# Kernel tuning notes

Measured on AMD Instinct MI355X. Metric: run time of the kernel, lower is better.

## Reference

```python
import math
import jax, jax.numpy as jnp
import numpy as np

D_MODEL = 1024
NUM_HEADS = 16
HEAD_DIM = D_MODEL // NUM_HEADS
B, T = 2, 2048


def setup_inputs() -> dict:
    key = jax.random.key(0)
    ks = jax.random.split(key, 11)
    s = 0.02
    inp = {
        'x':  jax.random.normal(ks[0], (B, T, D_MODEL), dtype=jnp.float32),
        'Wq': jax.random.normal(ks[1], (D_MODEL, D_MODEL), dtype=jnp.float32) * s,
        'bq': jax.random.normal(ks[2], (D_MODEL,), dtype=jnp.float32) * s,
        'Wk': jax.random.normal(ks[3], (D_MODEL, D_MODEL), dtype=jnp.float32) * s,
        'bk': jax.random.normal(ks[4], (D_MODEL,), dtype=jnp.float32) * s,
        'Wv': jax.random.normal(ks[5], (D_MODEL, D_MODEL), dtype=jnp.float32) * s,
        'bv': jax.random.normal(ks[6], (D_MODEL,), dtype=jnp.float32) * s,
        'Wt': jax.random.normal(ks[7], (D_MODEL, D_MODEL), dtype=jnp.float32) * s,
        'bt': jax.random.normal(ks[8], (D_MODEL,), dtype=jnp.float32) * s,
        'Wo': jax.random.normal(ks[9], (D_MODEL, D_MODEL), dtype=jnp.float32) * s,
        'bo': jax.random.normal(ks[10], (D_MODEL,), dtype=jnp.float32) * s,
    }
    return inp


def reference(x, Wq, bq, Wk, bk, Wv, bv, Wt, bt, Wo, bo):
    Bx, Tx, D = x.shape
    H, hd = NUM_HEADS, HEAD_DIM
    scale = 1.0 / math.sqrt(hd)

    def proj(W, b):
        # (B,T,D) -> (B,H,T,hd); torch Linear uses x @ W.T + b
        return (x @ W.T + b).reshape(Bx, Tx, H, hd).transpose(0, 2, 1, 3)

    q = proj(Wq, bq)
    k = proj(Wk, bk)
    v = proj(Wv, bv)
    t = proj(Wt, bt)

    # dot-product term: (B,H,T,T)
    scores = jnp.einsum('bhqd,bhkd->bhqk', q, k)
    # triplet term: cumsum over key positions of (k*v)/sqrt(hd)
    kv_cumsum = jnp.cumsum(k * v * scale, axis=2)  # (B,H,T,hd)
    scores = scores + jnp.einsum('bhqd,bhkd->bhqk', q * t, kv_cumsum)
    scores = scores * scale

    # causal mask: position j > i forbidden
    causal = jnp.tril(jnp.ones((Tx, Tx), dtype=bool))
    scores = jnp.where(causal[None, None], scores, jnp.float32(-jnp.inf))

    attn = jax.nn.softmax(scores, axis=-1)  # stable max-subtract internally
    out = jnp.einsum('bhqk,bhkd->bhqd', attn, v)
    out = out.transpose(0, 2, 1, 3).reshape(Bx, Tx, D)
    return out @ Wo.T + bo
```

## Files before the change

kernel.cpp:

```cpp
#include <hip/hip_runtime.h>
#include <hip/hip_bf16.h>

typedef unsigned short u16;
typedef __attribute__((ext_vector_type(8))) short bf16x8;
typedef __attribute__((ext_vector_type(4))) float f32x4;
typedef __attribute__((ext_vector_type(4))) unsigned int u32x4;

#define LOG2E 1.44269504088896340736f

static __device__ __forceinline__ float b2f(u16 u) {
    union { float f; unsigned int i; } v; v.i = ((unsigned int)u) << 16; return v.f;
}
static __device__ __forceinline__ u16 f2b(float f) {
    unsigned int x = __builtin_bit_cast(unsigned int, f);
    unsigned int r = (x + 0x7fffu + ((x >> 16) & 1u)) >> 16;
    return (u16)r;
}
static __device__ __forceinline__ void gll16(const u16* g, u16* l) {
    __builtin_amdgcn_global_load_lds((const __attribute__((address_space(1))) void*)g,
                                     (__attribute__((address_space(3))) void*)l, 16, 0, 0);
}
static __device__ __forceinline__ float fexp2(float x) {
    float r; asm("v_exp_f32 %0, %1" : "=v"(r) : "v"(x)); return r;
}

__global__ __launch_bounds__(256) void cvt_all(const float* __restrict__ x,
                                               const float* __restrict__ w0, const float* __restrict__ w1,
                                               const float* __restrict__ w2, const float* __restrict__ w3,
                                               const float* __restrict__ w4, u16* __restrict__ dst) {
    size_t c = (size_t)blockIdx.x * 256 + threadIdx.x;
    size_t e = c * 4;
    const float* s; size_t off;
    const size_t M4 = (size_t)4 << 20, M1 = (size_t)1 << 20;
    if (e < M4) { s = x; off = e; }
    else {
        size_t r = e - M4; int wsel = (int)(r >> 20); off = r & (M1 - 1);
        s = wsel == 0 ? w0 : wsel == 1 ? w1 : wsel == 2 ? w2 : wsel == 3 ? w3 : w4;
    }
    float4 v = *(const float4*)(s + off);
    u16* d = dst + e;
    d[0] = f2b(v.x); d[1] = f2b(v.y); d[2] = f2b(v.z); d[3] = f2b(v.w);
}

template<int WM>
static __device__ __forceinline__ void gemm_body(const u16* __restrict__ A, const u16* __restrict__ W,
                                                 const float* __restrict__ bias, void* __restrict__ outp,
                                                 int mode, u16* Al, u16* Bl, int tm, int tn) {
    const int tid = threadIdx.x, lane = tid & 63, w = tid >> 6;
    const int wr = w >> 1, wc = w & 1;
    const int l15 = lane & 15, lhi = lane >> 4;

    f32x4 acc[WM][4] = {};

    for (int kt = 0; kt < 16; ++kt) {
        const int k0 = kt * 64;
        #pragma unroll
        for (int i = 0; i < WM; ++i) {
            int rl = i * 32 + w * 8 + (lane >> 3);
            int c  = (lane & 7) ^ (rl & 7);
            gll16(A + (size_t)(tm + rl) * 1024 + k0 + c * 8, Al + (i * 32 + w * 8) * 64);
        }
        #pragma unroll
        for (int i = 0; i < 4; ++i) {
            int rl = i * 32 + w * 8 + (lane >> 3);
            int c  = (lane & 7) ^ (rl & 7);
            gll16(W + (size_t)(tn + rl) * 1024 + k0 + c * 8, Bl + (i * 32 + w * 8) * 64);
        }
        __syncthreads();
        #pragma unroll
        for (int ks = 0; ks < 2; ++ks) {
            bf16x8 af[WM], bfr[4];
            #pragma unroll
            for (int mi = 0; mi < WM; ++mi) {
                int row = wr * (WM * 16) + mi * 16 + l15;
                int cc = (ks * 4 + lhi) ^ (row & 7);
                af[mi] = *(const bf16x8*)(Al + row * 64 + cc * 8);
            }
            #pragma unroll
            for (int ni = 0; ni < 4; ++ni) {
                int row = wc * 64 + ni * 16 + l15;
                int cc = (ks * 4 + lhi) ^ (row & 7);
                bfr[ni] = *(const bf16x8*)(Bl + row * 64 + cc * 8);
            }
            #pragma unroll
            for (int mi = 0; mi < WM; ++mi)
                #pragma unroll
                for (int ni = 0; ni < 4; ++ni)
                    acc[mi][ni] = __builtin_amdgcn_mfma_f32_16x16x32_bf16(af[mi], bfr[ni], acc[mi][ni], 0, 0, 0);
        }
        __syncthreads();
    }

    float bcol[4];
    #pragma unroll
    for (int ni = 0; ni < 4; ++ni) bcol[ni] = bias[tn + wc * 64 + ni * 16 + l15];

    #pragma unroll
    for (int mi = 0; mi < WM; ++mi)
        #pragma unroll
        for (int ni = 0; ni < 4; ++ni)
            #pragma unroll
            for (int r = 0; r < 4; ++r) {
                int rg = tm + wr * (WM * 16) + mi * 16 + lhi * 4 + r;
                int cg = tn + wc * 64 + ni * 16 + l15;
                float v = acc[mi][ni][r] + bcol[ni];
                if (mode == 2) {
                    ((float*)outp)[(size_t)rg * 1024 + cg] = v;
                } else {
                    int b = rg >> 11, t = rg & 2047, h = cg >> 6, d = cg & 63;
                    if (mode == 0)
                        ((u16*)outp)[(((size_t)(b * 16 + h)) * 2048 + t) * 128 + d] = f2b(v);
                    else
                        ((u16*)outp)[(((size_t)(b * 16 + h)) * 2048 + t) * 64 + d] = f2b(v);
                }
            }
}

struct ProjArgs {
    const u16* W[4];
    const float* b[4];
    u16* out[4];
};

__global__ __launch_bounds__(256) void gemm_proj(const u16* __restrict__ A, ProjArgs pa) {
    __shared__ u16 Al[128 * 64];
    __shared__ u16 Bl[128 * 64];
    const int d = blockIdx.x + 8 * blockIdx.y + 256 * blockIdx.z;
    const int c = d & 7, wtn = d >> 3;
    const int z = c >> 1, yh = c & 1;
    const int yy = yh * 16 + (wtn >> 3);
    const int xx = wtn & 7;
    gemm_body<4>(A, pa.W[z], pa.b[z], pa.out[z], (z < 2) ? 0 : 1, Al, Bl, yy * 128, xx * 128);
}

__global__ __launch_bounds__(256) void gemm_out2(const u16* __restrict__ A, const u16* __restrict__ W,
                                                 const float* __restrict__ bias, void* __restrict__ out) {
    __shared__ u16 Al[64 * 64];
    __shared__ u16 Bl[128 * 64];
    const int d = blockIdx.x + 8 * blockIdx.y;
    const int c = d & 7, wtn = d >> 3;
    const int yy = c * 8 + (wtn >> 3);
    const int xx = wtn & 7;
    gemm_body<2>(A, W, bias, out, 2, Al, Bl, yy * 64, xx * 128);
}

__global__ __launch_bounds__(256) void fuse_small(u16* __restrict__ Qa, const u16* __restrict__ Tp,
                                                  const u16* __restrict__ V, u16* __restrict__ VT,
                                                  u16* __restrict__ Ka) {
    __shared__ char shmem[64 * 72 * 2];
    const int b = blockIdx.x, tid = threadIdx.x;

    if (b < 2048) {
        int idx = b * 256 + tid;
        int tg = idx >> 3, dc = idx & 7;
        bf16x8 q = *(const bf16x8*)(Qa + (size_t)tg * 128 + dc * 8);
        bf16x8 tt = *(const bf16x8*)(Tp + (size_t)tg * 64 + dc * 8);
        bf16x8 o;
        #pragma unroll
        for (int j = 0; j < 8; ++j) o[j] = (short)f2b(b2f((u16)q[j]) * b2f((u16)tt[j]));
        *(bf16x8*)(Qa + (size_t)tg * 128 + 64 + dc * 8) = o;
    } else if (b < 3072) {
        u16 (*tile)[72] = (u16(*)[72])shmem;
        const int r0 = b - 2048;
        const int bh = r0 >> 5, tc = r0 & 31;
        const u16* Vh = V + ((size_t)bh * 2048 + tc * 64) * 64;
        u16* VTh = VT + (size_t)bh * 64 * 2048 + tc * 64;
        for (int i = 0; i < 2; ++i) {
            int f = i * 256 + tid;
            int r = f >> 3, dc = f & 7;
            bf16x8 v = *(const bf16x8*)(Vh + r * 64 + dc * 8);
            #pragma unroll
            for (int j = 0; j < 8; ++j) tile[dc * 8 + j][r] = (u16)v[j];
        }
        __syncthreads();
        for (int i = 0; i < 2; ++i) {
            int f = i * 256 + tid;
            int d = f >> 3, t8 = (f & 7) * 8;
            bf16x8 o;
            #pragma unroll
            for (int j = 0; j < 8; ++j) {
                int pos = t8 + j;
                int key = (pos & 32) + 16 * ((pos >> 2) & 1) + 4 * ((pos >> 3) & 3) + (pos & 3);
                o[j] = (short)tile[d][key];
            }
            *(bf16x8*)(VTh + (size_t)d * 2048 + t8) = o;
        }
    } else {
        float4* sums = (float4*)shmem;
        const int r0 = b - 3072;
        const int bh = r0 & 31, dg = r0 >> 5;
        u16* Kh = Ka + (size_t)bh * 2048 * 128;
        const u16* Vh = V + (size_t)bh * 2048 * 64;
        const int quad = tid & 3, c = tid >> 2;
        const int d0 = dg * 16 + quad * 4;
        float s0 = 0.f, s1 = 0.f, s2 = 0.f, s3 = 0.f;
        for (int i = 0; i < 32; ++i) {
            int t = c * 32 + i;
            ushort4 kv = *(const ushort4*)(Kh + (size_t)t * 128 + d0);
            ushort4 vv = *(const ushort4*)(Vh + (size_t)t * 64 + d0);
            s0 += b2f(kv.x) * b2f(vv.x);
            s1 += b2f(kv.y) * b2f(vv.y);
            s2 += b2f(kv.z) * b2f(vv.z);
            s3 += b2f(kv.w) * b2f(vv.w);
        }
        float4 sv; sv.x = s0; sv.y = s1; sv.z = s2; sv.w = s3;
        sums[c * 4 + quad] = sv;
        __syncthreads();
        float4 run; run.x = run.y = run.z = run.w = 0.f;
        for (int cc = 0; cc < c; ++cc) {
            float4 ss = sums[cc * 4 + quad];
            run.x += ss.x; run.y += ss.y; run.z += ss.z; run.w += ss.w;
        }
        for (int i = 0; i < 32; ++i) {
            int t = c * 32 + i;
            ushort4 kv = *(const ushort4*)(Kh + (size_t)t * 128 + d0);
            ushort4 vv = *(const ushort4*)(Vh + (size_t)t * 64 + d0);
            run.x += b2f(kv.x) * b2f(vv.x);
            run.y += b2f(kv.y) * b2f(vv.y);
            run.z += b2f(kv.z) * b2f(vv.z);
            run.w += b2f(kv.w) * b2f(vv.w);
            ushort4 o;
            o.x = f2b(run.x * 0.125f); o.y = f2b(run.y * 0.125f);
            o.z = f2b(run.z * 0.125f); o.w = f2b(run.w * 0.125f);
            *(ushort4*)(Kh + (size_t)t * 128 + 64 + d0) = o;
        }
    }
}

__global__ __launch_bounds__(256, 3) void attn5(const u16* __restrict__ Qa, const u16* __restrict__ Ka,
                                                const u16* __restrict__ VT, u16* __restrict__ Obuf) {
    const int wg = blockIdx.x;
    const int xcd = wg & 7, slot = wg >> 3;
    const int bh = xcd * 4 + (slot >> 4);
    const int qp = slot & 15;
    const int tiL = qp, tiH = 31 - qp;
    const int q0L = tiL * 64, q0H = tiH * 64;
    const int NT = tiH + 1;
    const u16* Qh = Qa + (size_t)bh * 2048 * 128;
    const u16* Kh = Ka + (size_t)bh * 2048 * 128;
    const u16* VTh = VT + (size_t)bh * 64 * 2048;

    __shared__ u16 Kl[2][64 * 128];
    __shared__ u16 Vl[2][64 * 64];

    const int tid = threadIdx.x, lane = tid & 63, w = tid >> 6;
    const int l15 = lane & 15, lhi = lane >> 4;
    const float SC = 0.125f * LOG2E;

    bf16x8 qfL[4], qfH[4];
    #pragma unroll
    for (int ks = 0; ks < 4; ++ks) {
        bf16x8 a = *(const bf16x8*)(Qh + (size_t)(q0L + w * 16 + l15) * 128 + ks * 32 + lhi * 8);
        bf16x8 b = *(const bf16x8*)(Qh + (size_t)(q0H + w * 16 + l15) * 128 + ks * 32 + lhi * 8);
        bf16x8 oa, ob;
        #pragma unroll
        for (int j = 0; j < 8; ++j) {
            oa[j] = (short)f2b(b2f((u16)a[j]) * SC);
            ob[j] = (short)f2b(b2f((u16)b[j]) * SC);
        }
        qfL[ks] = oa; qfH[ks] = ob;
    }

    f32x4 accL[4] = {}, accH[4] = {};
    float lsL = 0.f, lsH = 0.f;

    auto STAGE = [&](int buf, int ti) {
        const int kv0 = ti * 64;
        #pragma unroll
        for (int i = 0; i < 4; ++i) {
            int lr = i * 16 + w * 4 + lhi;
            int c = l15 ^ (lr & 15);
            gll16(Kh + (size_t)(kv0 + lr) * 128 + c * 8, &Kl[buf][(i * 16 + w * 4) * 128]);
        }
        #pragma unroll
        for (int i = 0; i < 2; ++i) {
            int dr = i * 32 + w * 8 + (lane >> 3);
            int c = (lane & 7) ^ (dr & 7);
            gll16(VTh + (size_t)dr * 2048 + kv0 + c * 8, &Vl[buf][(i * 32 + w * 8) * 64]);
        }
    };

    STAGE(0, 0);
    asm volatile("s_waitcnt vmcnt(0)" ::: "memory");
    __builtin_amdgcn_s_barrier();

    for (int ti = 0; ti < NT; ++ti) {
        const int cur = ti & 1;
        if (ti + 1 < NT) STAGE(cur ^ 1, ti + 1);
        const bool doL = (ti <= tiL);

        f32x4 sH[4] = {}, sL[4] = {};
        #pragma unroll
        for (int ks = 0; ks < 4; ++ks) {
            bf16x8 kf[4];
            #pragma unroll
            for (int k2 = 0; k2 < 4; ++k2) {
                int kl = k2 * 16 + l15;
                int cc = (ks * 4 + lhi) ^ l15;
                kf[k2] = *(const bf16x8*)(&Kl[cur][kl * 128 + cc * 8]);
            }
            __builtin_amdgcn_s_setprio(1);
            #pragma unroll
            for (int k2 = 0; k2 < 4; ++k2)
                sH[k2] = __builtin_amdgcn_mfma_f32_16x16x32_bf16(kf[k2], qfH[ks], sH[k2], 0, 0, 0);
            if (doL) {
                #pragma unroll
                for (int k2 = 0; k2 < 4; ++k2)
                    sL[k2] = __builtin_amdgcn_mfma_f32_16x16x32_bf16(kf[k2], qfL[ks], sL[k2], 0, 0, 0);
            }
            __builtin_amdgcn_s_setprio(0);
        }

        auto FINISH = [&](f32x4* sacc, f32x4* acc, float& lsum, bool diag) {
            float p[4][4];
            #pragma unroll
            for (int k2 = 0; k2 < 4; ++k2)
                #pragma unroll
                for (int r = 0; r < 4; ++r) {
                    float s = sacc[k2][r];
                    if (diag) {
                        int key = k2 * 16 + lhi * 4 + r;
                        int qq = w * 16 + l15;
                        s = (key <= qq) ? s : -1e30f;
                    }
                    float pe = fexp2(s);
                    p[k2][r] = pe;
                    lsum += pe;
                }
            bf16x8 pf[2];
            #pragma unroll
            for (int ks2 = 0; ks2 < 2; ++ks2) {
                unsigned int w0, w1, w2, w3;
                asm("v_cvt_pk_bf16_f32 %0, %1, %2" : "=v"(w0) : "v"(p[2 * ks2][0]),     "v"(p[2 * ks2][1]));
                asm("v_cvt_pk_bf16_f32 %0, %1, %2" : "=v"(w1) : "v"(p[2 * ks2][2]),     "v"(p[2 * ks2][3]));
                asm("v_cvt_pk_bf16_f32 %0, %1, %2" : "=v"(w2) : "v"(p[2 * ks2 + 1][0]), "v"(p[2 * ks2 + 1][1]));
                asm("v_cvt_pk_bf16_f32 %0, %1, %2" : "=v"(w3) : "v"(p[2 * ks2 + 1][2]), "v"(p[2 * ks2 + 1][3]));
                u32x4 t = {w0, w1, w2, w3};
                pf[ks2] = __builtin_bit_cast(bf16x8, t);
            }
            #pragma unroll
            for (int ks2 = 0; ks2 < 2; ++ks2) {
                __builtin_amdgcn_s_setprio(1);
                #pragma unroll
                for (int dt = 0; dt < 4; ++dt) {
                    int dd = dt * 16 + l15;
                    int cc = (ks2 * 4 + lhi) ^ (dd & 7);
                    bf16x8 vf = *(const bf16x8*)(&Vl[cur][dd * 64 + cc * 8]);
                    acc[dt] = __builtin_amdgcn_mfma_f32_16x16x32_bf16(pf[ks2], vf, acc[dt], 0, 0, 0);
                }
                __builtin_amdgcn_s_setprio(0);
            }
        };

        FINISH(sH, accH, lsH, ti == tiH);
        if (doL) FINISH(sL, accL, lsL, ti == tiL);

        asm volatile("s_waitcnt vmcnt(0)" ::: "memory");
        __builtin_amdgcn_s_barrier();
    }

    lsH += __shfl_xor(lsH, 16, 64); lsH += __shfl_xor(lsH, 32, 64);
    lsL += __shfl_xor(lsL, 16, 64); lsL += __shfl_xor(lsL, 32, 64);
    float invH[4], invL[4];
    #pragma unroll
    for (int r = 0; r < 4; ++r) {
        invH[r] = 1.0f / __shfl(lsH, lhi * 4 + r, 64);
        invL[r] = 1.0f / __shfl(lsL, lhi * 4 + r, 64);
    }
    #pragma unroll
    for (int dt = 0; dt < 4; ++dt)
        #pragma unroll
        for (int r = 0; r < 4; ++r) {
            int cr = lhi * 4 + r;
            int dd = dt * 16 + l15;
            int qgL = q0L + w * 16 + cr;
            int qgH = q0H + w * 16 + cr;
            size_t nL = (size_t)(bh >> 4) * 2048 + qgL;
            size_t nH = (size_t)(bh >> 4) * 2048 + qgH;
            Obuf[nL * 1024 + (bh & 15) * 64 + dd] = f2b(accL[dt][r] * invL[r]);
            Obuf[nH * 1024 + (bh & 15) * 64 + dd] = f2b(accH[dt][r] * invH[r]);
        }
}

extern "C" void kernel_launch(void* const* d_in, const int* in_sizes, int n_in,
                              void* d_out, int out_size, void* d_ws, size_t ws_size,
                              hipStream_t stream) {
    (void)in_sizes; (void)n_in; (void)out_size; (void)ws_size;
    const float* x  = (const float*)d_in[0];
    const float* Wq = (const float*)d_in[1];
    const float* bq = (const float*)d_in[2];
    const float* Wk = (const float*)d_in[3];
    const float* bk = (const float*)d_in[4];
    const float* Wv = (const float*)d_in[5];
    const float* bv = (const float*)d_in[6];
    const float* Wt = (const float*)d_in[7];
    const float* bt = (const float*)d_in[8];
    const float* Wo = (const float*)d_in[9];
    const float* bo = (const float*)d_in[10];

    const size_t M1 = 1024u * 1024u;
    u16* xb   = (u16*)d_ws;
    u16* wq   = xb + 4 * M1;
    u16* wk   = wq + M1;
    u16* wv   = wk + M1;
    u16* wt   = wv + M1;
    u16* wo   = wt + M1;
    u16* Qa   = wo + M1;
    u16* Kaa  = Qa + 8 * M1;
    u16* Vtm  = Kaa + 8 * M1;
    u16* Ttm  = Vtm + 4 * M1;
    u16* Obuf = Ttm + 4 * M1;
    u16* VTg  = xb;

    cvt_all<<<9216, 256, 0, stream>>>(x, Wq, Wk, Wv, Wt, Wo, xb);

    ProjArgs pa;
    pa.W[0] = wq; pa.W[1] = wk; pa.W[2] = wv; pa.W[3] = wt;
    pa.b[0] = bq; pa.b[1] = bk; pa.b[2] = bv; pa.b[3] = bt;
    pa.out[0] = Qa; pa.out[1] = Kaa; pa.out[2] = Vtm; pa.out[3] = Ttm;
    gemm_proj<<<dim3(8, 32, 4), 256, 0, stream>>>(xb, pa);

    fuse_small<<<3200, 256, 0, stream>>>(Qa, Ttm, Vtm, VTg, Kaa);

    attn5<<<512, 256, 0, stream>>>(Qa, Kaa, VTg, Obuf);

    gemm_out2<<<dim3(8, 64), 256, 0, stream>>>(Obuf, wo, bo, d_out);
}
```

Measured before the change: 138.2 us.

## Split attention KV loop into two halves with a separate combine kernel

Each query-tile pair's KV loop is split across two workgroups, doubling the attention grid from 512 to 1024 blocks. Each half writes unnormalized bf16 partial outputs and per-row softmax denominators into reused workspace buffers. A new combine kernel sums the two partials, divides by the summed denominators and writes the final buffer. The aim is better CU occupancy and load balance during attention. In exchange it adds an extra launch, extra global traffic, and extra rounding from storing partials in bf16. The combine is only correct if the softmax uses a fixed rather than per-half running max.

```diff
diff --git a/kernel.cpp b/kernel.cpp
--- a/kernel.cpp
+++ b/kernel.cpp
@@ -227,18 +227,26 @@
     }
 }
 
-__global__ __launch_bounds__(256, 3) void attn5(const u16* __restrict__ Qa, const u16* __restrict__ Ka,
-                                                const u16* __restrict__ VT, u16* __restrict__ Obuf) {
+__global__ __launch_bounds__(256, 3) void attnSK(const u16* __restrict__ Qa, const u16* __restrict__ Ka,
+                                                 const u16* __restrict__ VT,
+                                                 u16* __restrict__ P0g, u16* __restrict__ P1g,
+                                                 float* __restrict__ Ls) {
     const int wg = blockIdx.x;
     const int xcd = wg & 7, slot = wg >> 3;
-    const int bh = xcd * 4 + (slot >> 4);
-    const int qp = slot & 15;
+    const int bh = xcd * 4 + (slot >> 5);
+    const int sub = slot & 31;
+    const int qp = sub & 15, half = sub >> 4;
     const int tiL = qp, tiH = 31 - qp;
     const int q0L = tiL * 64, q0H = tiH * 64;
     const int NT = tiH + 1;
+    const int mid = NT >> 1;
+    const int lo = half ? mid : 0;
+    const int hi = half ? NT : mid;
     const u16* Qh = Qa + (size_t)bh * 2048 * 128;
     const u16* Kh = Ka + (size_t)bh * 2048 * 128;
     const u16* VTh = VT + (size_t)bh * 64 * 2048;
+    u16* Pb = half ? P1g : P0g;
+    float* Lsb = Ls + (size_t)half * 32 * 2048;
 
     __shared__ u16 Kl[2][64 * 128];
     __shared__ u16 Vl[2][64 * 64];
@@ -280,13 +288,13 @@
         }
     };
 
-    STAGE(0, 0);
+    STAGE(lo & 1, lo);
     asm volatile("s_waitcnt vmcnt(0)" ::: "memory");
     __builtin_amdgcn_s_barrier();
 
-    for (int ti = 0; ti < NT; ++ti) {
+    for (int ti = lo; ti < hi; ++ti) {
         const int cur = ti & 1;
-        if (ti + 1 < NT) STAGE(cur ^ 1, ti + 1);
+        if (ti + 1 < hi) STAGE(cur ^ 1, ti + 1);
         const bool doL = (ti <= tiL);
 
         f32x4 sH[4] = {}, sL[4] = {};
@@ -361,12 +369,11 @@
 
     lsH += __shfl_xor(lsH, 16, 64); lsH += __shfl_xor(lsH, 32, 64);
     lsL += __shfl_xor(lsL, 16, 64); lsL += __shfl_xor(lsL, 32, 64);
-    float invH[4], invL[4];
-    #pragma unroll
-    for (int r = 0; r < 4; ++r) {
-        invH[r] = 1.0f / __shfl(lsH, lhi * 4 + r, 64);
-        invL[r] = 1.0f / __shfl(lsL, lhi * 4 + r, 64);
-    }
+    if (lhi == 0) {
+        Lsb[(size_t)bh * 2048 + q0H + w * 16 + l15] = lsH;
+        Lsb[(size_t)bh * 2048 + q0L + w * 16 + l15] = lsL;
+    }
+
     #pragma unroll
     for (int dt = 0; dt < 4; ++dt)
         #pragma unroll
@@ -377,9 +384,28 @@
             int qgH = q0H + w * 16 + cr;
             size_t nL = (size_t)(bh >> 4) * 2048 + qgL;
             size_t nH = (size_t)(bh >> 4) * 2048 + qgH;
-            Obuf[nL * 1024 + (bh & 15) * 64 + dd] = f2b(accL[dt][r] * invL[r]);
-            Obuf[nH * 1024 + (bh & 15) * 64 + dd] = f2b(accH[dt][r] * invH[r]);
-        }
+            Pb[nL * 1024 + (bh & 15) * 64 + dd] = f2b(accL[dt][r]);
+            Pb[nH * 1024 + (bh & 15) * 64 + dd] = f2b(accH[dt][r]);
+        }
+}
+
+__global__ __launch_bounds__(256) void combine_sk(const u16* __restrict__ P0g, const u16* __restrict__ P1g,
+                                                  const float* __restrict__ Ls, u16* __restrict__ Obuf) {
+    int idx = blockIdx.x * 256 + threadIdx.x;
+    size_t base = (size_t)idx * 8;
+    int n = (int)(base >> 10);
+    int col = (int)(base & 1023);
+    int b = n >> 11, q = n & 2047, h = col >> 6;
+    size_t bhq = (size_t)(b * 16 + h) * 2048 + q;
+    float l = Ls[bhq] + Ls[bhq + 32 * 2048];
+    float inv = 1.0f / l;
+    bf16x8 a = *(const bf16x8*)(P0g + base);
+    bf16x8 bb = *(const bf16x8*)(P1g + base);
+    bf16x8 o;
+    #pragma unroll
+    for (int j = 0; j < 8; ++j)
+        o[j] = (short)f2b((b2f((u16)a[j]) + b2f((u16)bb[j])) * inv);
+    *(bf16x8*)(Obuf + base) = o;
 }
 
 extern "C" void kernel_launch(void* const* d_in, const int* in_sizes, int n_in,
@@ -411,6 +437,9 @@
     u16* Ttm  = Vtm + 4 * M1;
     u16* Obuf = Ttm + 4 * M1;
     u16* VTg  = xb;
+    u16* P0g  = Vtm;
+    u16* P1g  = Ttm;
+    float* Ls = (float*)wq;
 
     cvt_all<<<9216, 256, 0, stream>>>(x, Wq, Wk, Wv, Wt, Wo, xb);
 
@@ -422,7 +451,8 @@
 
     fuse_small<<<3200, 256, 0, stream>>>(Qa, Ttm, Vtm, VTg, Kaa);
 
-    attn5<<<512, 256, 0, stream>>>(Qa, Kaa, VTg, Obuf);
+    attnSK<<<1024, 256, 0, stream>>>(Qa, Kaa, VTg, P0g, P1g, Ls);
+    combine_sk<<<2048, 256, 0, stream>>>(P0g, P1g, Ls, Obuf);
 
     gemm_out2<<<dim3(8, 64), 256, 0, stream>>>(Obuf, wo, bo, d_out);
 }
```

After: 142.5 us. 1.03x slower.
